# Optimization experiments

Hardware: AMD Instinct MI355X
Metric: run time of the kernel (lower is better)

Reference implementation:

```python
import jax, jax.numpy as jnp
import numpy as np
from jax import lax

EPS = 1e-4  # BatchNorm eps from the module
K = 3       # kernel_size
PAD = 1     # padding


def setup_inputs() -> dict:
    key = jax.random.key(0)
    k1, k2, k3 = jax.random.split(key, 3)
    N, Cin, H, Wd = 32, 256, 56, 56
    Cout = 256
    x = jax.random.normal(k1, (N, Cin, H, Wd), dtype=jnp.float32)
    gamma = jnp.ones((Cin,), dtype=jnp.float32)
    beta_bn = jnp.zeros((Cin,), dtype=jnp.float32)
    W = jax.random.normal(k2, (Cout, Cin, K, K), dtype=jnp.float32) * 0.05
    b = jax.random.normal(k3, (Cout,), dtype=jnp.float32) * 0.01
    return {"x": x, "gamma": gamma, "beta_bn": beta_bn, "W": W, "b": b}


def _conv(x, w, padding):
    return lax.conv_general_dilated(
        x, w, window_strides=(1, 1),
        padding=[(padding, padding), (padding, padding)],
        dimension_numbers=("NCHW", "OIHW", "NCHW"))


def reference(x, gamma, beta_bn, W, b):
    # BatchNorm2d in training mode: batch statistics over (N, H, W), biased var
    mu = jnp.mean(x, axis=(0, 2, 3), keepdims=True)
    var = jnp.var(x, axis=(0, 2, 3), keepdims=True)
    xn = (x - mu) * lax.rsqrt(var + EPS)
    xn = xn * gamma[None, :, None, None] + beta_bn[None, :, None, None]

    # BinActiv: per-pixel channel-mean of |x|, then sign-binarize
    m = jnp.mean(jnp.abs(xn), axis=1, keepdims=True)  # [N,1,H,W]
    xb = jnp.sign(xn)

    # Binarize weights; alpha = L1 norm per output filter / n
    n = W.shape[1] * W.shape[2] * W.shape[3]
    alpha = jnp.sum(jnp.abs(W), axis=(1, 2, 3)) / n  # [Cout]
    Wb = jnp.sign(W)

    y = _conv(xb, Wb, PAD) + b[None, :, None, None]

    # beta map: box filter (stride 1) over channel-mean magnitudes
    box = jnp.full((1, 1, K, K), 1.0 / (K * K), dtype=x.dtype)
    beta_map = _conv(m, box, PAD)  # [N,1,Ho,Wo]

    out = jax.nn.relu(y * beta_map * alpha[None, :, None, None])
    return out
```

## Files before the change

kernel.cpp:

```cpp
#include <hip/hip_runtime.h>
#include <cstdint>
#include <cstddef>

#define N_    32
#define C_    256
#define H_    56
#define W_    56
#define HW_   (H_ * W_)
#define NHW_  (N_ * HW_)
#define COUT_ 256
#define EPS_  1e-4f
#define PW_   58
#define PIMG_ (PW_ * PW_)

__global__ void k_bn_partial(const float* __restrict__ x,
                             float* __restrict__ ps, float* __restrict__ pq) {
    const int c = blockIdx.x >> 3;
    const int s = blockIdx.x & 7;
    const int t = threadIdx.x;
    float sm = 0.f, sq = 0.f;
    for (int n = s * 4; n < s * 4 + 4; ++n) {
        const float4* p = (const float4*)(x + (size_t)(n * C_ + c) * HW_);
        for (int i = t; i < HW_ / 4; i += 256) {
            float4 v = p[i];
            sm += v.x + v.y + v.z + v.w;
            sq += v.x * v.x + v.y * v.y + v.z * v.z + v.w * v.w;
        }
    }
    __shared__ float ls[256], lq[256];
    ls[t] = sm; lq[t] = sq;
    __syncthreads();
    for (int off = 128; off >= 1; off >>= 1) {
        if (t < off) { ls[t] += ls[t + off]; lq[t] += lq[t + off]; }
        __syncthreads();
    }
    if (t == 0) { ps[s * C_ + c] = ls[0]; pq[s * C_ + c] = lq[0]; }
}

__global__ void k_bn_final(const float* __restrict__ ps, const float* __restrict__ pq,
                           const float* __restrict__ gamma, const float* __restrict__ beta,
                           float* __restrict__ a, float* __restrict__ bb) {
    const int c = threadIdx.x;
    float sm = 0.f, sq = 0.f;
    for (int s = 0; s < 8; ++s) { sm += ps[s * C_ + c]; sq += pq[s * C_ + c]; }
    float mu   = sm * (1.f / NHW_);
    float var  = sq * (1.f / NHW_) - mu * mu;
    float rstd = rsqrtf(var + EPS_);
    float g    = gamma[c] * rstd;
    a[c]  = g;
    bb[c] = beta[c] - mu * g;
}

__global__ void k_wpack(const float* __restrict__ Wt, float* __restrict__ alpha,
                        uint64_t* __restrict__ wbits, int* __restrict__ ctab) {
    const int co = blockIdx.x;
    const int ci = threadIdx.x;
    const int lane = ci & 63, wave = ci >> 6;
    const float* p = Wt + (size_t)(co * C_ + ci) * 9;
    float wv[9];
    float asum = 0.f;
#pragma unroll
    for (int t = 0; t < 9; ++t) { wv[t] = p[t]; asum += fabsf(wv[t]); }
    __shared__ int Pl[9];
    if (ci < 9) Pl[ci] = 0;
    __syncthreads();
#pragma unroll
    for (int t = 0; t < 9; ++t) {
        uint64_t mask = __ballot(wv[t] > 0.f);
        if (lane == 0) {
            wbits[((size_t)co * 4 + wave) * 9 + t] = mask;
            atomicAdd(&Pl[t], (int)__popcll(mask));
        }
    }
    __shared__ float red[256];
    red[ci] = asum;
    __syncthreads();
    for (int off = 128; off >= 1; off >>= 1) {
        if (ci < off) red[ci] += red[ci + off];
        __syncthreads();
    }
    if (ci == 0) alpha[co] = red[0] * (1.f / 2304.f);
    if (ci < 9) {
        const int rc = ci / 3, cc = ci % 3;
        unsigned m9 = (rc == 0 ? 0x007u : 0u) | (rc == 2 ? 0x1C0u : 0u)
                    | (cc == 0 ? 0x049u : 0u) | (cc == 2 ? 0x124u : 0u);
        int s = 0;
#pragma unroll
        for (int t = 0; t < 9; ++t)
            if ((m9 >> t) & 1) s += 2 * Pl[t] - 256;
        ctab[ci * 256 + co] = s;
    }
}

__global__ void k_mpack(const float* __restrict__ x, const float* __restrict__ a,
                        const float* __restrict__ bb, uint64_t* __restrict__ xbits,
                        float* __restrict__ m) {
    const int p = blockIdx.x * 256 + threadIdx.x;
    const int wd = blockIdx.y;
    const int n = p / HW_;
    const int hw = p - n * HW_;
    const int h = hw / W_;
    const int w = hw - h * W_;
    const float* xp = x + (size_t)n * C_ * HW_ + (size_t)(wd * 64) * HW_ + hw;
    float macc = 0.f;
    uint64_t bw = 0;
#pragma unroll
    for (int j = 0; j < 64; ++j) {
        const int c = wd * 64 + j;
        float xn = fmaf(xp[(size_t)j * HW_], a[c], bb[c]);
        macc += fabsf(xn);
        bw |= (xn > 0.f) ? (1ull << j) : 0ull;
    }
    xbits[((size_t)wd * N_ + n) * PIMG_ + (size_t)(h + 1) * PW_ + (w + 1)] = bw;
    atomicAdd(&m[p], macc * (1.f / C_));
}

__global__ void k_box(const float* __restrict__ m, float* __restrict__ beta_map) {
    const int idx = blockIdx.x * 256 + threadIdx.x;
    if (idx >= NHW_) return;
    const int w = idx % W_;
    const int h = (idx / W_) % H_;
    const int n = idx / HW_;
    const float* mp = m + (size_t)n * HW_;
    float s = 0.f;
#pragma unroll
    for (int dh = 0; dh < 3; ++dh) {
        int ih = h + dh - 1;
        if (ih < 0 || ih >= H_) continue;
#pragma unroll
        for (int dw = 0; dw < 3; ++dw) {
            int iw = w + dw - 1;
            if (iw < 0 || iw >= W_) continue;
            s += mp[ih * W_ + iw];
        }
    }
    beta_map[idx] = s * (1.f / 9.f);
}

#define XNP(ACC, X64, W64) do {                                   \
    uint32_t _wl = (uint32_t)(W64), _wh = (uint32_t)((W64) >> 32); \
    uint32_t _xl = (uint32_t)(X64), _xh = (uint32_t)((X64) >> 32); \
    uint32_t _t0, _t1;                                             \
    asm("v_xor_b32 %0, %3, %5\n\t"                                 \
        "v_xor_b32 %1, %4, %6\n\t"                                 \
        "v_bcnt_u32_b32 %2, %0, %2\n\t"                            \
        "v_bcnt_u32_b32 %2, %1, %2"                                \
        : "=&v"(_t0), "=&v"(_t1), "+v"(ACC)                        \
        : "s"(_wl), "s"(_wh), "v"(_xl), "v"(_xh));                 \
} while (0)

__global__ void __launch_bounds__(256, 4)
k_conv(const uint64_t* __restrict__ xbits, const uint64_t* __restrict__ wbits,
       const int* __restrict__ ctab, const float* __restrict__ beta_map,
       const float* __restrict__ alpha, const float* __restrict__ bias,
       float* __restrict__ out) {
    const int p   = blockIdx.x * 256 + (int)threadIdx.x;
    const int grp = blockIdx.y;
    const int n  = p / HW_;
    const int hw = p - n * HW_;
    const int h  = hw / W_;
    const int w  = hw - h * W_;

    uint64_t xw[36];
#pragma unroll
    for (int wd = 0; wd < 4; ++wd) {
        const uint64_t* xp = xbits + ((size_t)wd * N_ + n) * PIMG_ + (size_t)h * PW_ + w;
#pragma unroll
        for (int r = 0; r < 3; ++r) {
            xw[wd * 9 + r * 3 + 0] = xp[r * PW_ + 0];
            xw[wd * 9 + r * 3 + 1] = xp[r * PW_ + 1];
            xw[wd * 9 + r * 3 + 2] = xp[r * PW_ + 2];
        }
    }

    const int rowcls = (h == 0) ? 0 : ((h == H_ - 1) ? 2 : 1);
    const int colcls = (w == 0) ? 0 : ((w == W_ - 1) ? 2 : 1);
    const int* crow = ctab + (rowcls * 3 + colcls) * 256 + grp * 64;
    const float bm = beta_map[p];
    float* op = out + (size_t)n * COUT_ * HW_ + (size_t)(grp * 64) * HW_ + hw;

#pragma unroll 1
    for (int coi = 0; coi < 64; ++coi) {
        const int co = grp * 64 + coi;
        const uint64_t* wr = wbits + (size_t)co * 36;
        int a0 = 0, a1 = 0, a2 = 0, a3 = 0;
#pragma unroll
        for (int k = 0; k < 9; ++k) {
            XNP(a0, xw[k],      wr[k]);
            XNP(a1, xw[9 + k],  wr[9 + k]);
            XNP(a2, xw[18 + k], wr[18 + k]);
            XNP(a3, xw[27 + k], wr[27 + k]);
        }
        const int acc = (a0 + a1) + (a2 + a3);
        const int dot = 2304 - 2 * acc + crow[coi];
        float o = ((float)dot + bias[co]) * bm * alpha[co];
        o = fmaxf(o, 0.f);
        op[(size_t)coi * HW_] = o;
    }
}

extern "C" void kernel_launch(void* const* d_in, const int* in_sizes, int n_in,
                              void* d_out, int out_size, void* d_ws, size_t ws_size,
                              hipStream_t stream) {
    (void)in_sizes; (void)n_in; (void)out_size; (void)ws_size;
    const float* x     = (const float*)d_in[0];
    const float* gamma = (const float*)d_in[1];
    const float* betab = (const float*)d_in[2];
    const float* Wt    = (const float*)d_in[3];
    const float* b     = (const float*)d_in[4];
    float* out = (float*)d_out;

    uint8_t* base = (uint8_t*)d_ws;
    float*    ps       = (float*)(base + 0);
    float*    pq       = (float*)(base + 8192);
    float*    a        = (float*)(base + 16384);
    float*    bb       = (float*)(base + 17408);
    float*    alpha    = (float*)(base + 18432);
    int*      ctab     = (int*)(base + 19456);
    uint64_t* wbits    = (uint64_t*)(base + 28672);
    uint64_t* xbits    = (uint64_t*)(base + 102400);
    float*    m        = (float*)(base + 3547136);
    float*    beta_map = (float*)(base + 3948544);

    k_bn_partial<<<2048, 256, 0, stream>>>(x, ps, pq);
    k_bn_final<<<1, 256, 0, stream>>>(ps, pq, gamma, betab, a, bb);
    k_wpack<<<COUT_, 256, 0, stream>>>(Wt, alpha, wbits, ctab);
    hipMemsetAsync(xbits, 0, (size_t)N_ * PIMG_ * 4 * sizeof(uint64_t), stream);
    hipMemsetAsync(m, 0, (size_t)NHW_ * sizeof(float), stream);
    k_mpack<<<dim3(NHW_ / 256, 4), 256, 0, stream>>>(x, a, bb, xbits, m);
    k_box<<<(NHW_ + 255) / 256, 256, 0, stream>>>(m, beta_map);
    k_conv<<<dim3(NHW_ / 256, 4), 256, 0, stream>>>(xbits, wbits, ctab, beta_map, alpha, b, out);
}
```

Before: 318.5 us.

## Restructure binary conv to accumulate 32 output channels per thread with transposed weights

The binary conv kernel now streams one 64-bit input word at a time and XNOR-popcounts it against 32 output channels held in register accumulators, instead of caching all 36 input words and looping over 64 output channels. The weight bit layout is transposed so the 32 channel weights for each (word, tap) pair are contiguous, which makes them uniform scalar loads. The grid doubles to 8 channel groups and the occupancy hint rises from 4 to 6 blocks per unit, trading a smaller register footprint for more parallelism. Each input word is reloaded once per group, so input reads grow, and the 32 accumulators all stay live until the output epilogue.

```diff
diff --git a/kernel.cpp b/kernel.cpp
--- a/kernel.cpp
+++ b/kernel.cpp
@@ -68,7 +68,7 @@
     for (int t = 0; t < 9; ++t) {
         uint64_t mask = __ballot(wv[t] > 0.f);
         if (lane == 0) {
-            wbits[((size_t)co * 4 + wave) * 9 + t] = mask;
+            wbits[((size_t)wave * 9 + t) * COUT_ + co] = mask;
             atomicAdd(&Pl[t], (int)__popcll(mask));
         }
     }
@@ -149,7 +149,7 @@
         : "s"(_wl), "s"(_wh), "v"(_xl), "v"(_xh));                 \
 } while (0)
 
-__global__ void __launch_bounds__(256, 4)
+__global__ void __launch_bounds__(256, 6)
 k_conv(const uint64_t* __restrict__ xbits, const uint64_t* __restrict__ wbits,
        const int* __restrict__ ctab, const float* __restrict__ beta_map,
        const float* __restrict__ alpha, const float* __restrict__ bias,
@@ -161,41 +161,39 @@
     const int h  = hw / W_;
     const int w  = hw - h * W_;
 
-    uint64_t xw[36];
-#pragma unroll
+    int acc[32];
+#pragma unroll
+    for (int i = 0; i < 32; ++i) acc[i] = 0;
+
+#pragma unroll 1
     for (int wd = 0; wd < 4; ++wd) {
         const uint64_t* xp = xbits + ((size_t)wd * N_ + n) * PIMG_ + (size_t)h * PW_ + w;
-#pragma unroll
+        const uint64_t* wbase = wbits + (size_t)wd * 9 * COUT_ + grp * 32;
+#pragma unroll 1
         for (int r = 0; r < 3; ++r) {
-            xw[wd * 9 + r * 3 + 0] = xp[r * PW_ + 0];
-            xw[wd * 9 + r * 3 + 1] = xp[r * PW_ + 1];
-            xw[wd * 9 + r * 3 + 2] = xp[r * PW_ + 2];
+#pragma unroll 1
+            for (int c = 0; c < 3; ++c) {
+                const uint64_t xv = xp[r * PW_ + c];
+                const uint64_t* wr = wbase + (r * 3 + c) * COUT_;
+#pragma unroll
+                for (int i = 0; i < 32; ++i) XNP(acc[i], xv, wr[i]);
+            }
         }
     }
 
     const int rowcls = (h == 0) ? 0 : ((h == H_ - 1) ? 2 : 1);
     const int colcls = (w == 0) ? 0 : ((w == W_ - 1) ? 2 : 1);
-    const int* crow = ctab + (rowcls * 3 + colcls) * 256 + grp * 64;
+    const int* crow = ctab + (rowcls * 3 + colcls) * 256 + grp * 32;
     const float bm = beta_map[p];
-    float* op = out + (size_t)n * COUT_ * HW_ + (size_t)(grp * 64) * HW_ + hw;
-
-#pragma unroll 1
-    for (int coi = 0; coi < 64; ++coi) {
-        const int co = grp * 64 + coi;
-        const uint64_t* wr = wbits + (size_t)co * 36;
-        int a0 = 0, a1 = 0, a2 = 0, a3 = 0;
-#pragma unroll
-        for (int k = 0; k < 9; ++k) {
-            XNP(a0, xw[k],      wr[k]);
-            XNP(a1, xw[9 + k],  wr[9 + k]);
-            XNP(a2, xw[18 + k], wr[18 + k]);
-            XNP(a3, xw[27 + k], wr[27 + k]);
-        }
-        const int acc = (a0 + a1) + (a2 + a3);
-        const int dot = 2304 - 2 * acc + crow[coi];
+    float* op = out + (size_t)n * COUT_ * HW_ + (size_t)(grp * 32) * HW_ + hw;
+
+#pragma unroll
+    for (int i = 0; i < 32; ++i) {
+        const int co = grp * 32 + i;
+        const int dot = 2304 - 2 * acc[i] + crow[i];
         float o = ((float)dot + bias[co]) * bm * alpha[co];
         o = fmaxf(o, 0.f);
-        op[(size_t)coi * HW_] = o;
+        op[(size_t)i * HW_] = o;
     }
 }
 
@@ -229,5 +227,5 @@
     hipMemsetAsync(m, 0, (size_t)NHW_ * sizeof(float), stream);
     k_mpack<<<dim3(NHW_ / 256, 4), 256, 0, stream>>>(x, a, bb, xbits, m);
     k_box<<<(NHW_ + 255) / 256, 256, 0, stream>>>(m, beta_map);
-    k_conv<<<dim3(NHW_ / 256, 4), 256, 0, stream>>>(xbits, wbits, ctab, beta_map, alpha, b, out);
-}
+    k_conv<<<dim3(NHW_ / 256, 8), 256, 0, stream>>>(xbits, wbits, ctab, beta_map, alpha, b, out);
+}
```

Result: no change. 320.1 us (+0.5%).

## Stream input bit-words per tap instead of caching 36 in registers

Applied to the files above, without the earlier changes.

The conv kernel no longer holds all 36 packed input words in registers. It loops over output channels in chunks of 8 and reloads each input tap word from memory per chunk, accumulating 8 channels at once. The weight bit layout is transposed so that the 8 consecutive output channels for a tap are contiguous, which allows vectorized scalar loads. Launch bounds rise to 8 waves per SIMD to cut register pressure and raise occupancy, at the cost of 8x more input loads, which rely on the cache.

```diff
diff --git a/kernel.cpp b/kernel.cpp
--- a/kernel.cpp
+++ b/kernel.cpp
@@ -68,7 +68,7 @@
     for (int t = 0; t < 9; ++t) {
         uint64_t mask = __ballot(wv[t] > 0.f);
         if (lane == 0) {
-            wbits[((size_t)co * 4 + wave) * 9 + t] = mask;
+            wbits[((size_t)wave * 9 + t) * COUT_ + co] = mask;
             atomicAdd(&Pl[t], (int)__popcll(mask));
         }
     }
@@ -149,7 +149,7 @@
         : "s"(_wl), "s"(_wh), "v"(_xl), "v"(_xh));                 \
 } while (0)
 
-__global__ void __launch_bounds__(256, 4)
+__global__ void __launch_bounds__(256, 8)
 k_conv(const uint64_t* __restrict__ xbits, const uint64_t* __restrict__ wbits,
        const int* __restrict__ ctab, const float* __restrict__ beta_map,
        const float* __restrict__ alpha, const float* __restrict__ bias,
@@ -161,18 +161,6 @@
     const int h  = hw / W_;
     const int w  = hw - h * W_;
 
-    uint64_t xw[36];
-#pragma unroll
-    for (int wd = 0; wd < 4; ++wd) {
-        const uint64_t* xp = xbits + ((size_t)wd * N_ + n) * PIMG_ + (size_t)h * PW_ + w;
-#pragma unroll
-        for (int r = 0; r < 3; ++r) {
-            xw[wd * 9 + r * 3 + 0] = xp[r * PW_ + 0];
-            xw[wd * 9 + r * 3 + 1] = xp[r * PW_ + 1];
-            xw[wd * 9 + r * 3 + 2] = xp[r * PW_ + 2];
-        }
-    }
-
     const int rowcls = (h == 0) ? 0 : ((h == H_ - 1) ? 2 : 1);
     const int colcls = (w == 0) ? 0 : ((w == W_ - 1) ? 2 : 1);
     const int* crow = ctab + (rowcls * 3 + colcls) * 256 + grp * 64;
@@ -180,22 +168,34 @@
     float* op = out + (size_t)n * COUT_ * HW_ + (size_t)(grp * 64) * HW_ + hw;
 
 #pragma unroll 1
-    for (int coi = 0; coi < 64; ++coi) {
-        const int co = grp * 64 + coi;
-        const uint64_t* wr = wbits + (size_t)co * 36;
-        int a0 = 0, a1 = 0, a2 = 0, a3 = 0;
-#pragma unroll
-        for (int k = 0; k < 9; ++k) {
-            XNP(a0, xw[k],      wr[k]);
-            XNP(a1, xw[9 + k],  wr[9 + k]);
-            XNP(a2, xw[18 + k], wr[18 + k]);
-            XNP(a3, xw[27 + k], wr[27 + k]);
-        }
-        const int acc = (a0 + a1) + (a2 + a3);
-        const int dot = 2304 - 2 * acc + crow[coi];
-        float o = ((float)dot + bias[co]) * bm * alpha[co];
-        o = fmaxf(o, 0.f);
-        op[(size_t)coi * HW_] = o;
+    for (int ch = 0; ch < 8; ++ch) {
+        int acc[8];
+#pragma unroll
+        for (int i = 0; i < 8; ++i) acc[i] = 0;
+
+#pragma unroll 1
+        for (int wd = 0; wd < 4; ++wd) {
+            const uint64_t* xp = xbits + ((size_t)wd * N_ + n) * PIMG_
+                                       + (size_t)h * PW_ + w;
+            const uint64_t* wq = wbits + (size_t)wd * 9 * COUT_ + grp * 64 + ch * 8;
+#pragma unroll 3
+            for (int t = 0; t < 9; ++t) {
+                const uint64_t xv = *(const volatile uint64_t*)(xp + (t / 3) * PW_ + (t % 3));
+                const uint64_t* wr = wq + t * COUT_;
+#pragma unroll
+                for (int i = 0; i < 8; ++i) XNP(acc[i], xv, wr[i]);
+            }
+        }
+
+#pragma unroll
+        for (int i = 0; i < 8; ++i) {
+            const int coi = ch * 8 + i;
+            const int co  = grp * 64 + coi;
+            const int dot = 2304 - 2 * acc[i] + crow[coi];
+            float o = ((float)dot + bias[co]) * bm * alpha[co];
+            o = fmaxf(o, 0.f);
+            op[(size_t)coi * HW_] = o;
+        }
     }
 }
 
```

After: 359.5 us. 1.13x slower.
